# Performance work log

Measured on AMD Instinct MI355X. Metric: run time of the kernel, lower is better.

## Reference

```python
import jax, jax.numpy as jnp
import numpy as np

T, B, S, D = 512, 32, 512, 512
EPS = 1e-6  # LayerNorm eps


def _ln(x, g, b):
    m = jnp.mean(x, axis=-1, keepdims=True)
    v = jnp.mean((x - m) ** 2, axis=-1, keepdims=True)
    return g * (x - m) * jax.lax.rsqrt(v + EPS) + b


def setup_inputs() -> dict:
    key = jax.random.key(0)
    ks = jax.random.split(key, 10)
    sc = 1.0 / np.sqrt(D).astype(np.float32)
    return {
        "prev_layer": jax.random.normal(ks[0], (T, B, D), jnp.float32),
        "hidden": jax.random.normal(ks[1], (B, D), jnp.float32),
        "enc_output": jax.random.normal(ks[2], (B, S, D), jnp.float32),
        "memory_length": jax.random.randint(ks[3], (B,), 1, S + 1),
        # nn.Linear weights stored as [in, out] (transposed torch layout)
        "W_in": jax.random.normal(ks[4], (D, 3 * D), jnp.float32) * sc,
        "W_enc": jax.random.normal(ks[5], (D, D), jnp.float32) * sc,
        "W_attn_in": jax.random.normal(ks[6], (D, D), jnp.float32) * sc,
        "W_hidden": jax.random.normal(ks[7], (D, D), jnp.float32) * sc,
        "W_ctx": jax.random.normal(ks[8], (D, D), jnp.float32) * sc,
        # LayerNorm gains/biases (5 LNs)
        "g_pre": jnp.ones((3 * D,), jnp.float32), "b_pre": jnp.zeros((3 * D,), jnp.float32),
        "g_enc": jnp.ones((D,), jnp.float32), "b_enc": jnp.zeros((D,), jnp.float32),
        "g_attn": jnp.ones((D,), jnp.float32), "b_attn": jnp.zeros((D,), jnp.float32),
        "g_h": jnp.ones((D,), jnp.float32), "b_h": jnp.zeros((D,), jnp.float32),
        "g_c": jnp.ones((D,), jnp.float32), "b_c": jnp.zeros((D,), jnp.float32),
    }


def reference(prev_layer, hidden, enc_output, W_in, W_enc, W_attn_in, W_hidden,
              W_ctx, g_pre, b_pre, g_enc, b_enc, g_attn, b_attn, g_h, b_h,
              g_c, b_c, memory_length):
    d = prev_layer.shape[-1]
    sqrt_d = jnp.sqrt(jnp.asarray(d, prev_layer.dtype))
    # dropout is identity in eval mode
    preact = _ln(prev_layer @ W_in, g_pre, b_pre)          # [T,B,3D]
    pctx = _ln(enc_output @ W_enc, g_enc, b_enc)           # [B,S,D]
    z, h_gate, pl_t = jnp.split(preact, 3, axis=-1)
    z = jax.nn.sigmoid(z)
    h_gate = jax.nn.sigmoid(h_gate)

    # SRU-style linear recurrence: s_t = (1-z_t)*s_{t-1} + z_t*pl_t
    def step(h, zp):
        z_t, p_t = zp
        s = (1.0 - z_t) * h + z_t * p_t
        return s, s

    hidden_last, ss = jax.lax.scan(step, hidden, (z, pl_t))  # ss: [T,B,D]

    attn_in = _ln(ss @ W_attn_in, g_attn, b_attn)            # [T,B,D]
    align = jnp.einsum('tbd,bsd->bts', attn_in, pctx)        # [B,T,S]
    mask = jnp.arange(pctx.shape[1])[None, :] < memory_length[:, None]  # [B,S]
    align = jnp.where(mask[:, None, :], align, -jnp.inf)
    av = jax.nn.softmax(align / sqrt_d, axis=-1)             # [B,T,S]
    c = jnp.einsum('bts,bsd->tbd', av, pctx)                 # [T,B,D]
    attn_out = c / sqrt_d

    trans = _ln(ss @ W_hidden, g_h, b_h) + _ln(attn_out @ W_ctx, g_c, b_c)
    out = jnp.tanh(trans)
    out = (1.0 - h_gate) * out + h_gate * prev_layer         # [T,B,D]
    p_attn = jnp.transpose(av, (1, 0, 2))                    # [T,B,S]
    return out, hidden_last, p_attn
```

## Files before the change

kernel.cpp:

```cpp
#include <hip/hip_runtime.h>
#include <hip/hip_bf16.h>
#include <cmath>

#define T_ 512
#define B_ 32
#define S_ 512
#define D_ 512
#define NCH 16
#define CT (T_ / NCH)
static constexpr float LN_EPS = 1e-6f;
static constexpr float RSQRT_D = 0.044194173824159216f;

typedef __attribute__((ext_vector_type(8))) __bf16 bf16x8;
typedef __attribute__((ext_vector_type(4))) float f32x4;

struct __align__(8) bfx4 { __hip_bfloat16 x, y, z, w; };
struct __align__(16) u16x8 { unsigned short h[8]; };

__device__ __forceinline__ void g2l16(const void* g, void* l) {
    __builtin_amdgcn_global_load_lds(
        (const __attribute__((address_space(1))) unsigned int*)g,
        (__attribute__((address_space(3))) unsigned int*)l, 16, 0, 0);
}

__device__ __forceinline__ float xr_sum16(float v) {
    v += __shfl_xor(v, 1); v += __shfl_xor(v, 2);
    v += __shfl_xor(v, 4); v += __shfl_xor(v, 8); return v;
}
__device__ __forceinline__ float xr_max16(float v) {
    v = fmaxf(v, __shfl_xor(v, 1)); v = fmaxf(v, __shfl_xor(v, 2));
    v = fmaxf(v, __shfl_xor(v, 4)); v = fmaxf(v, __shfl_xor(v, 8)); return v;
}

__device__ __forceinline__ float sigmoidf_(float x) {
    return 1.f / (1.f + __expf(-x));
}
__device__ __forceinline__ float sigmoid_fast(float x) {
    return __fdividef(1.f, 1.f + __expf(-x));
}
__device__ __forceinline__ float tanh_fast(float x) {
    return 1.f - __fdividef(2.f, __expf(2.f * x) + 1.f);
}
__device__ __forceinline__ float bfu(unsigned short u) {
    unsigned int v = ((unsigned int)u) << 16;
    return __uint_as_float(v);
}
__device__ __forceinline__ unsigned short f2bu(float f) {
    return __hip_bfloat16_raw(__float2bfloat16(f)).x;
}

__device__ __forceinline__ void g128_body(
    const __hip_bfloat16* __restrict__ A, long ldaE,
    const __hip_bfloat16* __restrict__ Bw,
    __hip_bfloat16* __restrict__ out, long outStrideB,
    float2* __restrict__ part, int partMul, int partBase,
    float scale, int bx, int by)
{
    __shared__ char smem[49152];
    const int m0 = by * 128, n0 = bx * 128;
    const int tid = threadIdx.x, lane = tid & 63, w = tid >> 6;
    const int wm = (w >> 1) * 64, wn = (w & 1) * 64;
    const int srow = lane >> 2, skB = (lane & 3) * 16;
    const int q = lane >> 4, c = lane & 15;

    f32x4 acc[4][4];
#pragma unroll
    for (int i = 0; i < 4; i++)
#pragma unroll
        for (int j = 0; j < 4; j++) acc[i][j] = (f32x4)(0.0f);

    const char* ga0 = (const char*)(A + (long)(m0 + w * 16 + srow) * ldaE) + skB;
    const char* ga1 = (const char*)(A + (long)(m0 + (w + 4) * 16 + srow) * ldaE) + skB;
    const char* gb0 = (const char*)(Bw + (long)(n0 + w * 16 + srow) * 512) + skB;
    const char* gb1 = (const char*)(Bw + (long)(n0 + (w + 4) * 16 + srow) * 512) + skB;
    char* la0 = smem + w * 1024 + lane * 16;
    char* la1 = smem + (w + 4) * 1024 + lane * 16;
    char* lb0 = smem + 8192 + w * 1024 + lane * 16;
    char* lb1 = smem + 8192 + (w + 4) * 1024 + lane * 16;
    const char* Ar = smem + (wm + c) * 64 + q * 16;
    const char* Br = smem + 8192 + (wn + c) * 64 + q * 16;

    g2l16(ga0, la0);
    g2l16(ga1, la1);
    g2l16(gb0, lb0);
    g2l16(gb1, lb1);
    g2l16(ga0 + 64, la0 + 16384);
    g2l16(ga1 + 64, la1 + 16384);
    g2l16(gb0 + 64, lb0 + 16384);
    g2l16(gb1 + 64, lb1 + 16384);
    asm volatile("s_waitcnt vmcnt(4)" ::: "memory");
    __builtin_amdgcn_s_barrier();
    __builtin_amdgcn_sched_barrier(0);

#pragma unroll
    for (int kk = 0; kk < 16; kk++) {
        const int cb = (kk % 3) * 16384;
        if (kk < 14) {
            const int nb = ((kk + 2) % 3) * 16384;
            const long kb = (long)(kk + 2) * 64;
            g2l16(ga0 + kb, la0 + nb);
            g2l16(ga1 + kb, la1 + nb);
            g2l16(gb0 + kb, lb0 + nb);
            g2l16(gb1 + kb, lb1 + nb);
        }
        bf16x8 af[4], bfr[4];
#pragma unroll
        for (int i = 0; i < 4; i++) {
            af[i] = *(const bf16x8*)(Ar + cb + i * 1024);
            bfr[i] = *(const bf16x8*)(Br + cb + i * 1024);
        }
#pragma unroll
        for (int i = 0; i < 4; i++)
#pragma unroll
            for (int j = 0; j < 4; j++)
                acc[i][j] = __builtin_amdgcn_mfma_f32_16x16x32_bf16(
                    af[i], bfr[j], acc[i][j], 0, 0, 0);
        if (kk < 15) {
            if (kk < 14)
                asm volatile("s_waitcnt vmcnt(4) lgkmcnt(0)" ::: "memory");
            else
                asm volatile("s_waitcnt vmcnt(0) lgkmcnt(0)" ::: "memory");
            __builtin_amdgcn_s_barrier();
            __builtin_amdgcn_sched_barrier(0);
        }
    }
    __syncthreads();

    if (part) {
        float2* sred = (float2*)smem;
#pragma unroll
        for (int i = 0; i < 4; i++)
#pragma unroll
            for (int r = 0; r < 4; r++) {
                float s = 0.f, qq = 0.f;
#pragma unroll
                for (int j = 0; j < 4; j++) {
                    float v = acc[i][j][r] * scale; s += v; qq += v * v;
                }
                s = xr_sum16(s); qq = xr_sum16(qq);
                if (c == 0) sred[(wm + i * 16 + q * 4 + r) * 2 + (w & 1)] =
                    make_float2(s, qq);
            }
        __syncthreads();
        if ((w & 1) == 0 && c == 0) {
#pragma unroll
            for (int i = 0; i < 4; i++)
#pragma unroll
                for (int r = 0; r < 4; r++) {
                    int row = wm + i * 16 + q * 4 + r;
                    float2 a = sred[row * 2], b2 = sred[row * 2 + 1];
                    part[(long)bx * 16384 + (long)(m0 + row) * partMul + partBase] =
                        make_float2(a.x + b2.x, a.y + b2.y);
                }
        }
        __syncthreads();
    }

    for (int p = 0; p < 2; p++) {
        if ((w >> 1) == p) {
#pragma unroll
            for (int i = 0; i < 4; i++)
#pragma unroll
                for (int j = 0; j < 4; j++)
#pragma unroll
                    for (int r = 0; r < 4; r++) {
                        int row = i * 16 + q * 4 + r;
                        int col = wn + j * 16 + c;
                        ((__hip_bfloat16*)smem)[row * 128 + col] =
                            __float2bfloat16(acc[i][j][r] * scale);
                    }
        }
        __syncthreads();
#pragma unroll
        for (int rnd = 0; rnd < 4; rnd++) {
            int row = rnd * 16 + (tid >> 4);
            int ch = tid & 15;
            uint4 v = *(const uint4*)(smem + row * 256 + ch * 16);
            long grow = m0 + p * 64 + row;
            *(uint4*)((char*)out + grow * outStrideB + (long)n0 * 2 + ch * 16) = v;
        }
        __syncthreads();
    }
}

__global__ __launch_bounds__(256) void g128(
    const __hip_bfloat16* __restrict__ A, long ldaE,
    const __hip_bfloat16* __restrict__ Bw, long bStrideZ,
    __hip_bfloat16* __restrict__ out, long outStrideB,
    float2* __restrict__ part, float scale, int swizzle)
{
    int bx, by, pmul = 1, pbase = 0;
    if (gridDim.z > 1) {
        bx = blockIdx.x; by = blockIdx.y;
        A += (long)blockIdx.z * 512;
        Bw += (long)blockIdx.z * bStrideZ;
        out += (long)blockIdx.z * 512;
        pmul = 32; pbase = blockIdx.z;
    } else if (swizzle) {
        const int nwg = gridDim.x * gridDim.y;
        const int lin = blockIdx.y * gridDim.x + blockIdx.x;
        const int cpx = nwg >> 3;
        const int swz = (lin & 7) * cpx + (lin >> 3);
        bx = swz % gridDim.x; by = swz / gridDim.x;
    } else { bx = blockIdx.x; by = blockIdx.y; }
    g128_body(A, ldaE, Bw, out, outStrideB, part, pmul, pbase, scale, bx, by);
}

__global__ __launch_bounds__(256) void g128e2s(
    const __hip_bfloat16* __restrict__ encb,
    const __hip_bfloat16* __restrict__ WE2,
    __hip_bfloat16* __restrict__ E2, float2* __restrict__ partA,
    const __hip_bfloat16* __restrict__ preb, const float2* __restrict__ stats,
    const float* __restrict__ gpre, const float* __restrict__ bpre,
    float* __restrict__ Ap, float* __restrict__ Bp)
{
    const int bid = blockIdx.x;
    if (bid < 512) {
        int i2 = (bid & 31) * 256 + threadIdx.x;
        int b = i2 >> 8, d = (i2 & 255) * 2;
        int idx = b * 512 + d;
        int ch = bid >> 5;
        float2 gz = *(const float2*)(gpre + d), bz = *(const float2*)(bpre + d);
        float2 gp = *(const float2*)(gpre + 1024 + d);
        float2 bp = *(const float2*)(bpre + 1024 + d);
        float A0 = 1.f, s0 = 0.f, A1 = 1.f, s1 = 0.f;
        for (int t = ch * CT; t < (ch + 1) * CT; t++) {
            long row = (long)t * 32 + b;
            float2 st = stats[row];
            ushort2 zr = *(const ushort2*)(preb + row * 1536 + d);
            ushort2 pr = *(const ushort2*)(preb + row * 1536 + 1024 + d);
            float z0 = sigmoidf_((bfu(zr.x) - st.x) * st.y * gz.x + bz.x);
            float z1 = sigmoidf_((bfu(zr.y) - st.x) * st.y * gz.y + bz.y);
            float p0 = (bfu(pr.x) - st.x) * st.y * gp.x + bp.x;
            float p1 = (bfu(pr.y) - st.x) * st.y * gp.y + bp.y;
            A0 *= (1.f - z0); s0 = (1.f - z0) * s0 + z0 * p0;
            A1 *= (1.f - z1); s1 = (1.f - z1) * s1 + z1 * p1;
        }
        *(float2*)(Ap + ch * 16384 + idx) = make_float2(A0, A1);
        *(float2*)(Bp + ch * 16384 + idx) = make_float2(s0, s1);
        return;
    }
    const int local = bid - 512;
    const int swz = (local & 7) * 128 + (local >> 3);
    g128_body(encb, 512, WE2, E2, 2048, partA, 1, 0, 1.f, swz & 7, swz >> 3);
}

__global__ __launch_bounds__(256) void mfix3(
    const __hip_bfloat16* __restrict__ preb, const float2* __restrict__ stats,
    const float* __restrict__ gpre, const float* __restrict__ bpre,
    const float* __restrict__ sinb, __hip_bfloat16* __restrict__ ssb,
    const __hip_bfloat16* __restrict__ E2,
    __hip_bfloat16* __restrict__ pctxb, __hip_bfloat16* __restrict__ pwT,
    const float2* __restrict__ partA,
    const float* __restrict__ g, const float* __restrict__ bb,
    const float* __restrict__ uv)
{
    __shared__ __hip_bfloat16 t[32][34];
    __shared__ float2 sst[32];
    const int bid = blockIdx.x;
    if (bid < 512) {
        int i2 = (bid & 31) * 256 + threadIdx.x;
        int b = i2 >> 8, d = (i2 & 255) * 2;
        int idx = b * 512 + d;
        int ch = bid >> 5;
        float2 gz = *(const float2*)(gpre + d), bz = *(const float2*)(bpre + d);
        float2 gp = *(const float2*)(gpre + 1024 + d);
        float2 bp = *(const float2*)(bpre + 1024 + d);
        float2 sv = *(const float2*)(sinb + ch * 16384 + idx);
        float s0 = sv.x, s1 = sv.y;
        for (int tt = ch * CT; tt < (ch + 1) * CT; tt++) {
            long row = (long)tt * 32 + b;
            float2 st = stats[row];
            ushort2 zr = *(const ushort2*)(preb + row * 1536 + d);
            ushort2 pr = *(const ushort2*)(preb + row * 1536 + 1024 + d);
            float z0 = sigmoidf_((bfu(zr.x) - st.x) * st.y * gz.x + bz.x);
            float z1 = sigmoidf_((bfu(zr.y) - st.x) * st.y * gz.y + bz.y);
            float p0 = (bfu(pr.x) - st.x) * st.y * gp.x + bp.x;
            float p1 = (bfu(pr.y) - st.x) * st.y * gp.y + bp.y;
            s0 += z0 * (p0 - s0);
            s1 += z1 * (p1 - s1);
            ushort2 o;
            o.x = f2bu(s0); o.y = f2bu(s1);
            *(ushort2*)(ssb + (long)tt * 16384 + idx) = o;
        }
        return;
    }
    const int local = bid - 512;
    const int d0 = (local & 15) * 32;
    const int s0 = ((local >> 4) & 15) * 32;
    const int b = local >> 8;
    if (threadIdx.x < 32) {
        long row = (long)b * 512 + s0 + threadIdx.x;
        float s = 0.f, qq = 0.f;
#pragma unroll
        for (int cb = 0; cb < 4; cb++) {
            float2 v = partA[(long)cb * 16384 + row]; s += v.x; qq += v.y;
        }
        float mn = s * (1.f / 512);
        sst[threadIdx.x] =
            make_float2(mn, rsqrtf(qq * (1.f / 512) - mn * mn + LN_EPS));
    }
    __syncthreads();
    const int tx = threadIdx.x & 31, ty = threadIdx.x >> 5;
    const float gv = g[d0 + tx], bv = bb[d0 + tx];
    const float ud = uv[d0 + tx], vd = uv[512 + d0 + tx];
#pragma unroll
    for (int i = 0; i < 4; i++) {
        int srow = s0 + ty + i * 8;
        long row = (long)b * 512 + srow;
        float2 s = sst[ty + i * 8];
        float pc = __bfloat162float(E2[row * 1024 + d0 + tx]);
        pctxb[row * 512 + d0 + tx] =
            __float2bfloat16((pc - s.x) * s.y * gv + bv);
        float pr = __bfloat162float(E2[row * 1024 + 512 + d0 + tx]);
        t[ty + i * 8][tx] = __float2bfloat16(s.y * pr - s.y * s.x * ud + vd);
    }
    __syncthreads();
#pragma unroll
    for (int i = 0; i < 4; i++)
        pwT[(long)b * 262144 + (long)(d0 + ty + i * 8) * 512 + s0 + tx] =
            t[tx][ty + i * 8];
}

#define RC_BUF 34816
__global__ __launch_bounds__(256, 2) void gemm_attn(
    const __hip_bfloat16* __restrict__ attninC2,
    const __hip_bfloat16* __restrict__ pctxb,
    const float2* __restrict__ partB,
    const float* __restrict__ g_att, const float* __restrict__ b_att,
    const int* __restrict__ mlen,
    float* __restrict__ pattn, __hip_bfloat16* __restrict__ softb)
{
    __shared__ char smem[74240];
    float2* sst = (float2*)(smem + 69632);
    float* gln = (float*)(smem + 69888);
    float* bln = (float*)(smem + 71936);
    const int b = blockIdx.z;
    const long t0 = (long)blockIdx.y * 32;
    const int tid = threadIdx.x, lane = tid & 63, w = tid >> 6;

    if (tid < 32) {
        long grow = (t0 + tid) * 32 + b;
        float s = 0.f, qq = 0.f;
#pragma unroll
        for (int cb = 0; cb < 4; cb++) {
            float2 v = partB[(long)cb * 16384 + grow]; s += v.x; qq += v.y;
        }
        float mn = s * (1.f / 512);
        sst[tid] = make_float2(mn, rsqrtf(qq * (1.f / 512) - mn * mn + LN_EPS));
    }
    gln[tid] = g_att[tid]; gln[256 + tid] = g_att[256 + tid];
    bln[tid] = b_att[tid]; bln[256 + tid] = b_att[256 + tid];

    f32x4 acc[2][8];
#pragma unroll
    for (int m = 0; m < 2; m++)
#pragma unroll
        for (int j = 0; j < 8; j++) acc[m][j] = (f32x4)(0.0f);

    const __hip_bfloat16* A = attninC2 + (long)b * 1024 + t0 * 32768;
    const __hip_bfloat16* Bm = pctxb + (long)b * 262144;
    const char* ga = (const char*)(A + (long)(w * 16 + (lane >> 2)) * 32768) + (lane & 3) * 16;
    char* la = smem + w * 1024 + lane * 16;
    const char* gb = (const char*)(Bm + (long)(w * 128 + (lane >> 2)) * 512) + (lane & 3) * 16;
    char* lb = smem + 2048 + w * 8192 + lane * 16;
    const long ldbB16 = 512L * 32;
    const char* Ar = smem + (lane & 15) * 64 + (lane >> 4) * 16;
    const char* Br = smem + 2048 + (w * 128 + (lane & 15)) * 64 + (lane >> 4) * 16;

    if (w < 2) g2l16(ga, la);
#pragma unroll
    for (int s = 0; s < 8; s++) g2l16(gb + s * ldbB16, lb + s * 1024);
    __syncthreads();

    const int fr = lane & 15, kq = lane >> 4;
    const float2 st0 = sst[fr], st1 = sst[16 + fr];

#pragma unroll
    for (int kk = 0; kk < 16; kk++) {
        const int cb = (kk & 1) * RC_BUF;
        const int nb = ((kk & 1) ^ 1) * RC_BUF;
        if (kk < 15) {
            const long kb = (long)(kk + 1) * 64;
            if (w < 2) g2l16(ga + kb, la + nb);
#pragma unroll
            for (int s = 0; s < 8; s++)
                g2l16(gb + kb + s * ldbB16, lb + nb + s * 1024);
        }
        bf16x8 af[2], bfr[8];
#pragma unroll
        for (int m = 0; m < 2; m++) af[m] = *(const bf16x8*)(Ar + cb + m * 1024);
#pragma unroll
        for (int j = 0; j < 8; j++) bfr[j] = *(const bf16x8*)(Br + cb + j * 1024);
        {
            const int k0 = kk * 32 + kq * 8;
            float4 gq0 = *(const float4*)(gln + k0);
            float4 gq1 = *(const float4*)(gln + k0 + 4);
            float4 bq0 = *(const float4*)(bln + k0);
            float4 bq1 = *(const float4*)(bln + k0 + 4);
            float gj[8] = {gq0.x, gq0.y, gq0.z, gq0.w, gq1.x, gq1.y, gq1.z, gq1.w};
            float bj[8] = {bq0.x, bq0.y, bq0.z, bq0.w, bq1.x, bq1.y, bq1.z, bq1.w};
            u16x8 u0 = __builtin_bit_cast(u16x8, af[0]);
            u16x8 u1 = __builtin_bit_cast(u16x8, af[1]);
#pragma unroll
            for (int j = 0; j < 8; j++) {
                u0.h[j] = f2bu((bfu(u0.h[j]) - st0.x) * st0.y * gj[j] + bj[j]);
                u1.h[j] = f2bu((bfu(u1.h[j]) - st1.x) * st1.y * gj[j] + bj[j]);
            }
            af[0] = __builtin_bit_cast(bf16x8, u0);
            af[1] = __builtin_bit_cast(bf16x8, u1);
        }
#pragma unroll
        for (int m = 0; m < 2; m++)
#pragma unroll
            for (int j = 0; j < 8; j++)
                acc[m][j] = __builtin_amdgcn_mfma_f32_16x16x32_bf16(
                    af[m], bfr[j], acc[m][j], 0, 0, 0);
        __syncthreads();
    }

    const int q = lane >> 4, c = lane & 15;
    const int len = mlen[b];
    float* sred = (float*)smem;

#pragma unroll
    for (int m = 0; m < 2; m++)
#pragma unroll
        for (int r = 0; r < 4; r++) {
            float mx = -INFINITY;
#pragma unroll
            for (int j = 0; j < 8; j++) {
                int col = w * 128 + j * 16 + c;
                float v = acc[m][j][r] * RSQRT_D;
                acc[m][j][r] = v;
                if (col < len) mx = fmaxf(mx, v);
            }
            mx = xr_max16(mx);
            if (c == 0) sred[(m * 16 + q * 4 + r) * 4 + w] = mx;
        }
    __syncthreads();
    float rmax[2][4];
#pragma unroll
    for (int m = 0; m < 2; m++)
#pragma unroll
        for (int r = 0; r < 4; r++) {
            int row = m * 16 + q * 4 + r;
            rmax[m][r] = fmaxf(fmaxf(sred[row * 4], sred[row * 4 + 1]),
                               fmaxf(sred[row * 4 + 2], sred[row * 4 + 3]));
        }
    __syncthreads();
#pragma unroll
    for (int m = 0; m < 2; m++)
#pragma unroll
        for (int r = 0; r < 4; r++) {
            float s = 0.f;
#pragma unroll
            for (int j = 0; j < 8; j++) {
                int col = w * 128 + j * 16 + c;
                float e = (col < len) ? __expf(acc[m][j][r] - rmax[m][r]) : 0.f;
                acc[m][j][r] = e; s += e;
            }
            s = xr_sum16(s);
            if (c == 0) sred[(m * 16 + q * 4 + r) * 4 + w] = s;
        }
    __syncthreads();
    float rinv[2][4];
#pragma unroll
    for (int m = 0; m < 2; m++)
#pragma unroll
        for (int r = 0; r < 4; r++) {
            int row = m * 16 + q * 4 + r;
            rinv[m][r] = 1.f / (sred[row * 4] + sred[row * 4 + 1] +
                                sred[row * 4 + 2] + sred[row * 4 + 3]);
        }
    __syncthreads();

#pragma unroll
    for (int m = 0; m < 2; m++)
#pragma unroll
        for (int j = 0; j < 8; j++)
#pragma unroll
            for (int r = 0; r < 4; r++) {
                int row = m * 16 + q * 4 + r;
                int col = w * 128 + j * 16 + c;
                float p = acc[m][j][r] * rinv[m][r];
                pattn[((t0 + row) * 32 + b) * 512 + col] = p;
                ((__hip_bfloat16*)smem)[row * 512 + col] = __float2bfloat16(p);
            }
    __syncthreads();
#pragma unroll
    for (int rnd = 0; rnd < 8; rnd++) {
        int row = rnd * 4 + w;
        uint4 v = *(const uint4*)(smem + row * 1024 + lane * 16);
        *(uint4*)((char*)softb + ((t0 + row) * 32 + b) * 1024 + lane * 16) = v;
    }
}

__global__ __launch_bounds__(256) void fin_ep(
    const __hip_bfloat16* __restrict__ h2r,
    const __hip_bfloat16* __restrict__ C2,
    const __hip_bfloat16* __restrict__ preb,
    const float2* __restrict__ partC,
    const float2* __restrict__ partH,
    const float2* __restrict__ st_p,
    const float* __restrict__ g_c, const float* __restrict__ b_c,
    const float* __restrict__ g_h, const float* __restrict__ b_h,
    const float* __restrict__ g_pre, const float* __restrict__ b_pre,
    const float* __restrict__ prev, float* __restrict__ out)
{
    __shared__ float2 shc[32], shh[32];
    const long m0 = (long)blockIdx.x * 32;
    const int tid = threadIdx.x;
    if (tid < 32) {
        long rowg = m0 + tid;
        float s = 0.f, qq = 0.f;
#pragma unroll
        for (int cb = 0; cb < 4; cb++) {
            float2 v = partC[(long)cb * 16384 + rowg]; s += v.x; qq += v.y;
        }
        float mn = s * (1.f / 512);
        shc[tid] = make_float2(mn, rsqrtf(qq * (1.f / 512) - mn * mn + LN_EPS));
    } else if (tid < 64) {
        long rowg = m0 + tid - 32;
        float s = 0.f, qq = 0.f;
#pragma unroll
        for (int cb = 0; cb < 4; cb++) {
            float2 v = partH[(long)cb * 16384 + rowg]; s += v.x; qq += v.y;
        }
        float mn = s * (1.f / 512);
        shh[tid - 32] = make_float2(mn, rsqrtf(qq * (1.f / 512) - mn * mn + LN_EPS));
    }
    __syncthreads();
#pragma unroll
    for (int ch = 0; ch < 16; ch++) {
        int f4 = ch * 256 + tid;
        int row = f4 >> 7;
        long rowg = m0 + row;
        int col = (f4 & 127) * 4;
        ushort4 h2 = *(const ushort4*)((const char*)h2r + rowg * 1024 + col * 2);
        ushort4 h1 = *(const ushort4*)((const char*)C2 + rowg * 2048 + 1024 + col * 2);
        ushort4 hr = *(const ushort4*)((const char*)preb + rowg * 3072 + 1024 + col * 2);
        float4 pv = *(const float4*)(prev + rowg * 512 + col);
        float4 gc = *(const float4*)(g_c + col), bc = *(const float4*)(b_c + col);
        float4 gh = *(const float4*)(g_h + col), bh = *(const float4*)(b_h + col);
        float4 gp = *(const float4*)(g_pre + 512 + col);
        float4 bp = *(const float4*)(b_pre + 512 + col);
        float2 sc = shc[row], sh = shh[row], sp = st_p[rowg];
        auto fuse = [&](unsigned short h2u, unsigned short h1u, unsigned short hru,
                        float pvv, float gcv, float bcv, float ghv, float bhv,
                        float gpv, float bpv) -> float {
            float t2 = (bfu(h2u) - sc.x) * sc.y * gcv + bcv;
            float t1 = (bfu(h1u) - sh.x) * sh.y * ghv + bhv;
            float hg = sigmoid_fast((bfu(hru) - sp.x) * sp.y * gpv + bpv);
            return (1.f - hg) * tanh_fast(t1 + t2) + hg * pvv;
        };
        float4 o;
        o.x = fuse(h2.x, h1.x, hr.x, pv.x, gc.x, bc.x, gh.x, bh.x, gp.x, bp.x);
        o.y = fuse(h2.y, h1.y, hr.y, pv.y, gc.y, bc.y, gh.y, bh.y, gp.y, bp.y);
        o.z = fuse(h2.z, h1.z, hr.z, pv.z, gc.z, bc.z, gh.z, bh.z, gp.z, bp.z);
        o.w = fuse(h2.w, h1.w, hr.w, pv.w, gc.w, bc.w, gh.w, bh.w, gp.w, bp.w);
        *(float4*)(out + rowg * 512 + col) = o;
    }
}

__global__ __launch_bounds__(256) void cvt4d(
    const float* __restrict__ a, __hip_bfloat16* __restrict__ ya,
    const float* __restrict__ b, __hip_bfloat16* __restrict__ yb)
{
    int i = blockIdx.x * 256 + threadIdx.x;
    const float* x; __hip_bfloat16* y; int k;
    if (i < 2097152) { x = a; y = ya; k = i; }
    else { x = b; y = yb; k = i - 2097152; }
    float4 v = ((const float4*)x)[k];
    bfx4 o;
    o.x = __float2bfloat16(v.x); o.y = __float2bfloat16(v.y);
    o.z = __float2bfloat16(v.z); o.w = __float2bfloat16(v.w);
    ((bfx4*)y)[k] = o;
}

__global__ __launch_bounds__(256) void wtrans(
    const float* __restrict__ w0, const float* __restrict__ w1,
    const float* __restrict__ w2, const float* __restrict__ w3,
    const float* __restrict__ w4, __hip_bfloat16* __restrict__ WT,
    __hip_bfloat16* __restrict__ WE2)
{
    int z = blockIdx.z;
    const float* W; __hip_bfloat16* O; int N;
    if (z == 0)      { W = w0; O = WT;                          N = 1536; }
    else if (z == 1) { W = w1; O = WE2;                         N = 512; }
    else if (z == 2) { W = w2; O = WT + 786432 + 262144;        N = 512; }
    else if (z == 3) { W = w3; O = WT + 786432 + 524288;        N = 512; }
    else             { W = w4; O = WT + 786432 + 786432;        N = 512; }
    int n0 = blockIdx.x * 32, k0 = blockIdx.y * 32;
    if (n0 >= N) return;
    __shared__ float t[32][33];
    int tx = threadIdx.x & 31, ty = threadIdx.x >> 5;
#pragma unroll
    for (int i = 0; i < 4; i++)
        t[ty + i * 8][tx] = W[(long)(k0 + ty + i * 8) * N + n0 + tx];
    __syncthreads();
#pragma unroll
    for (int i = 0; i < 4; i++)
        O[(long)(n0 + ty + i * 8) * 512 + k0 + tx] =
            __float2bfloat16(t[tx][ty + i * 8]);
}

__global__ __launch_bounds__(256) void wprep(
    const __hip_bfloat16* __restrict__ wctxT, const float* __restrict__ g,
    __hip_bfloat16* __restrict__ wgT,
    const float* __restrict__ Wenc, __hip_bfloat16* __restrict__ wencb,
    const float* __restrict__ Wctx, const float* __restrict__ bvec,
    float* __restrict__ uv)
{
    const int bid = blockIdx.x;
    if (bid < 1024) {
        int i = bid * 256 + threadIdx.x;
        int d1 = i & 511;
        wgT[i] = __float2bfloat16(__bfloat162float(wctxT[i]) * g[d1]);
    } else if (bid < 1280) {
        int i = (bid - 1024) * 256 + threadIdx.x;
        float4 v = ((const float4*)Wenc)[i];
        bfx4 o;
        o.x = __float2bfloat16(v.x); o.y = __float2bfloat16(v.y);
        o.z = __float2bfloat16(v.z); o.w = __float2bfloat16(v.w);
        ((bfx4*)wencb)[i] = o;
    } else {
        int d = (bid - 1280) * 256 + threadIdx.x;
        float u = 0.f, v = 0.f;
        for (int k = 0; k < 512; k++) {
            float w = Wctx[(long)k * 512 + d];
            u += g[k] * w; v += bvec[k] * w;
        }
        uv[d] = u; uv[512 + d] = v;
    }
}

__global__ __launch_bounds__(256) void stats_fin(
    const float2* __restrict__ part, float2* __restrict__ stats)
{
    int r = blockIdx.x * 256 + threadIdx.x;
    float s = 0.f, qq = 0.f;
#pragma unroll
    for (int cb = 0; cb < 12; cb++) {
        float2 v = part[(long)cb * 16384 + r]; s += v.x; qq += v.y;
    }
    float m = s * (1.f / 1536);
    float rs = rsqrtf(qq * (1.f / 1536) - m * m + LN_EPS);
    stats[r] = make_float2(m, rs);
}

__global__ __launch_bounds__(256) void scan_part2(
    const float* __restrict__ Ap, const float* __restrict__ Bp,
    const float* __restrict__ h0, float* __restrict__ sin_,
    float* __restrict__ hlast)
{
    int idx = blockIdx.x * 256 + threadIdx.x;
    float s = h0[idx];
    for (int ch = 0; ch < NCH; ch++) {
        sin_[ch * 16384 + idx] = s;
        s = Ap[ch * 16384 + idx] * s + Bp[ch * 16384 + idx];
    }
    hlast[idx] = s;
}

extern "C" void kernel_launch(void* const* d_in, const int* in_sizes, int n_in,
                              void* d_out, int out_size, void* d_ws, size_t ws_size,
                              hipStream_t stream) {
    const float* prev  = (const float*)d_in[0];
    const float* hid0  = (const float*)d_in[1];
    const float* enc   = (const float*)d_in[2];
    const int*   mlen  = (const int*)  d_in[3];
    const float* W_in  = (const float*)d_in[4];
    const float* W_enc = (const float*)d_in[5];
    const float* W_att = (const float*)d_in[6];
    const float* W_hid = (const float*)d_in[7];
    const float* W_ctx = (const float*)d_in[8];
    const float* g_pre = (const float*)d_in[9];
    const float* b_pre = (const float*)d_in[10];
    const float* g_enc = (const float*)d_in[11];
    const float* b_enc = (const float*)d_in[12];
    const float* g_att = (const float*)d_in[13];
    const float* b_att = (const float*)d_in[14];
    const float* g_h   = (const float*)d_in[15];
    const float* b_h   = (const float*)d_in[16];
    const float* g_c   = (const float*)d_in[17];
    const float* b_c   = (const float*)d_in[18];

    float* out   = (float*)d_out;
    float* hlast = out + (long)T_ * B_ * D_;
    float* pattn = hlast + (long)B_ * D_;

    char* ws = (char*)d_ws;
    __hip_bfloat16* preb    = (__hip_bfloat16*)(ws);
    __hip_bfloat16* WT      = (__hip_bfloat16*)(ws + 50331648);
    __hip_bfloat16* prevb   = (__hip_bfloat16*)(ws + 54525952);
    __hip_bfloat16* encb    = (__hip_bfloat16*)(ws + 71303168);
    __hip_bfloat16* pctxb   = (__hip_bfloat16*)(ws + 88080384);
    __hip_bfloat16* pwT     = (__hip_bfloat16*)(ws + 104857600);
    __hip_bfloat16* ssb     = (__hip_bfloat16*)(ws + 121634816);
    __hip_bfloat16* C2      = (__hip_bfloat16*)(ws + 138412032);
    __hip_bfloat16* E2      = (__hip_bfloat16*)(ws + 171966464);
    __hip_bfloat16* softb   = (__hip_bfloat16*)(ws + 171966464);
    __hip_bfloat16* h2raw   = (__hip_bfloat16*)(ws + 188743680);
    float2* part            = (float2*)(ws + 205520896);
    float2* stats           = (float2*)(ws + 207618048);
    float* scanA            = (float*)(ws + 207749120);
    float* scanB            = (float*)(ws + 208797696);
    float* sinb             = (float*)(ws + 209846272);
    __hip_bfloat16* WE2     = (__hip_bfloat16*)(ws + 211419136);
    float* uv               = (float*)(ws + 212467712);
    __hip_bfloat16* WgT     = (__hip_bfloat16*)scanA;
    __hip_bfloat16* Wencbf  = (__hip_bfloat16*)scanB;

    float2* partA = part;
    float2* partB = part + 8 * 16384;
    float2* partC = part;

    const __hip_bfloat16* W_attT = WT + 786432 + 262144;
    const __hip_bfloat16* W_ctxT = WT + 786432 + 786432;

    dim3 blk(256);

    cvt4d<<<16384, blk, 0, stream>>>(prev, prevb, enc, encb);
    wtrans<<<dim3(48, 16, 5), blk, 0, stream>>>(W_in, W_enc, W_att, W_hid,
                                                W_ctx, WT, WE2);
    wprep<<<1282, blk, 0, stream>>>(W_ctxT, g_enc, WgT, W_enc, Wencbf,
                                    W_ctx, b_enc, uv);
    g128<<<dim3(4, 4), blk, 0, stream>>>(WgT, 512, Wencbf, 0, WE2 + 262144,
                                         1024, nullptr, 1.f, 0);

    g128<<<dim3(12, 128), blk, 0, stream>>>(prevb, 512, WT, 0, preb, 3072,
                                            part, 1.f, 1);
    stats_fin<<<64, blk, 0, stream>>>(part, stats);

    g128e2s<<<1536, blk, 0, stream>>>(encb, WE2, E2, partA, preb, stats,
                                      g_pre, b_pre, scanA, scanB);
    scan_part2<<<64, blk, 0, stream>>>(scanA, scanB, hid0, sinb, hlast);

    mfix3<<<8704, blk, 0, stream>>>(preb, stats, g_pre, b_pre, sinb, ssb,
                                    E2, pctxb, pwT, partA, g_enc, b_enc, uv);

    g128<<<dim3(8, 128), blk, 0, stream>>>(ssb, 512, W_attT, 0, C2, 2048,
                                           partB, 1.f, 1);

    gemm_attn<<<dim3(1, 16, 32), blk, 0, stream>>>(C2, pctxb, partB,
                                                   g_att, b_att, mlen,
                                                   pattn, softb);

    g128<<<dim3(4, 4, 32), blk, 0, stream>>>(softb, 16384, pwT, 262144,
                                             h2raw, 32768, partC, RSQRT_D, 0);

    fin_ep<<<512, blk, 0, stream>>>(h2raw, C2, preb, partC,
                                    partB + 4 * 16384, stats,
                                    g_c, b_c, g_h, b_h, g_pre, b_pre, prev,
                                    out);
}
```

Before: 488.4 us.

## Switch GEMM to double-buffered LDS pipeline and XCD-swizzle batched/attention grids

```diff
diff --git a/kernel.cpp b/kernel.cpp
--- a/kernel.cpp
+++ b/kernel.cpp
@@ -56,7 +56,7 @@
     float2* __restrict__ part, int partMul, int partBase,
     float scale, int bx, int by)
 {
-    __shared__ char smem[49152];
+    __shared__ char smem[32768];
     const int m0 = by * 128, n0 = bx * 128;
     const int tid = threadIdx.x, lane = tid & 63, w = tid >> 6;
     const int wm = (w >> 1) * 64, wn = (w & 1) * 64;
@@ -84,20 +84,14 @@
     g2l16(ga1, la1);
     g2l16(gb0, lb0);
     g2l16(gb1, lb1);
-    g2l16(ga0 + 64, la0 + 16384);
-    g2l16(ga1 + 64, la1 + 16384);
-    g2l16(gb0 + 64, lb0 + 16384);
-    g2l16(gb1 + 64, lb1 + 16384);
-    asm volatile("s_waitcnt vmcnt(4)" ::: "memory");
-    __builtin_amdgcn_s_barrier();
-    __builtin_amdgcn_sched_barrier(0);
+    __syncthreads();
 
 #pragma unroll
     for (int kk = 0; kk < 16; kk++) {
-        const int cb = (kk % 3) * 16384;
-        if (kk < 14) {
-            const int nb = ((kk + 2) % 3) * 16384;
-            const long kb = (long)(kk + 2) * 64;
+        const int cb = (kk & 1) << 14;
+        const int nb = cb ^ 16384;
+        if (kk < 15) {
+            const long kb = (long)(kk + 1) * 64;
             g2l16(ga0 + kb, la0 + nb);
             g2l16(ga1 + kb, la1 + nb);
             g2l16(gb0 + kb, lb0 + nb);
@@ -115,16 +109,8 @@
             for (int j = 0; j < 4; j++)
                 acc[i][j] = __builtin_amdgcn_mfma_f32_16x16x32_bf16(
                     af[i], bfr[j], acc[i][j], 0, 0, 0);
-        if (kk < 15) {
-            if (kk < 14)
-                asm volatile("s_waitcnt vmcnt(4) lgkmcnt(0)" ::: "memory");
-            else
-                asm volatile("s_waitcnt vmcnt(0) lgkmcnt(0)" ::: "memory");
-            __builtin_amdgcn_s_barrier();
-            __builtin_amdgcn_sched_barrier(0);
-        }
-    }
-    __syncthreads();
+        __syncthreads();
+    }
 
     if (part) {
         float2* sred = (float2*)smem;
@@ -191,11 +177,17 @@
 {
     int bx, by, pmul = 1, pbase = 0;
     if (gridDim.z > 1) {
-        bx = blockIdx.x; by = blockIdx.y;
-        A += (long)blockIdx.z * 512;
-        Bw += (long)blockIdx.z * bStrideZ;
-        out += (long)blockIdx.z * 512;
-        pmul = 32; pbase = blockIdx.z;
+        const int bpz = gridDim.x * gridDim.y;
+        const int nwg = bpz * gridDim.z;
+        const int lin = (blockIdx.z * gridDim.y + blockIdx.y) * gridDim.x
+                        + blockIdx.x;
+        const int swz = (lin & 7) * (nwg >> 3) + (lin >> 3);
+        const int z = swz / bpz, rem = swz % bpz;
+        bx = rem % gridDim.x; by = rem / gridDim.x;
+        A += (long)z * 512;
+        Bw += (long)z * bStrideZ;
+        out += (long)z * 512;
+        pmul = 32; pbase = z;
     } else if (swizzle) {
         const int nwg = gridDim.x * gridDim.y;
         const int lin = blockIdx.y * gridDim.x + blockIdx.x;
@@ -335,8 +327,10 @@
     float2* sst = (float2*)(smem + 69632);
     float* gln = (float*)(smem + 69888);
     float* bln = (float*)(smem + 71936);
-    const int b = blockIdx.z;
-    const long t0 = (long)blockIdx.y * 32;
+    const int lin = blockIdx.z * 16 + blockIdx.y;
+    const int swzb = (lin & 7) * 64 + (lin >> 3);
+    const int b = swzb >> 4;
+    const long t0 = (long)(swzb & 15) * 32;
     const int tid = threadIdx.x, lane = tid & 63, w = tid >> 6;
 
     if (tid < 32) {
```

Result: faster. 421.6 us (-13.7%).
